# Performance work log

Hardware: AMD Instinct MI355X
Metric: run time of the kernel (lower is better)

## Reference

```python
import jax, jax.numpy as jnp
import numpy as np

N_HEAD = 32
N_QUERY_GROUPS = 8
HEAD_SIZE = 128
N_EMBD = 4096


def apply_rope(x, cos, sin):
    # x: [B, H, T, D]; cos/sin: [T, D] (rotary_percentage = 1.0 so D = head_size)
    d = x.shape[-1]
    x1, x2 = x[..., : d // 2], x[..., d // 2:]
    rotated = jnp.concatenate([-x2, x1], axis=-1)
    return x * cos + rotated * sin


def setup_inputs() -> dict:
    key = jax.random.key(0)
    k1, k2, k3, k4, k5 = jax.random.split(key, 5)
    B, T = 1, 2048
    x = jax.random.normal(k1, (B, T, N_EMBD), dtype=jnp.float32)
    # realistic rope angles
    theta = 10000.0 ** (-jnp.arange(0, HEAD_SIZE // 2, dtype=jnp.float32) * 2.0 / HEAD_SIZE)
    ang = jnp.arange(T, dtype=jnp.float32)[:, None] * theta[None, :]
    ang = jnp.concatenate([ang, ang], axis=-1)  # [T, HEAD_SIZE]
    cos, sin = jnp.cos(ang), jnp.sin(ang)
    qkv_dim = (N_HEAD + 2 * N_QUERY_GROUPS) * HEAD_SIZE  # 6144
    w_attn = jax.random.normal(k2, (qkv_dim, N_EMBD), dtype=jnp.float32) * (N_EMBD ** -0.5)
    w_proj = jax.random.normal(k3, (N_EMBD, N_HEAD * HEAD_SIZE), dtype=jnp.float32) * ((N_HEAD * HEAD_SIZE) ** -0.5)
    return {"x": x, "cos": cos, "sin": sin, "w_attn": w_attn, "w_proj": w_proj}


def reference(x, cos, sin, w_attn, w_proj):
    B, T, C = x.shape
    G, hs = N_QUERY_GROUPS, HEAD_SIZE
    q_per_kv = N_HEAD // G  # 4
    total_qkv = q_per_kv + 2

    qkv = jnp.einsum('btc,oc->bto', x, w_attn)  # [B, T, 6144]
    qkv = qkv.reshape(B, T, G, total_qkv, hs).transpose(0, 2, 3, 1, 4)  # [B, G, total, T, hs]
    q = qkv[:, :, :q_per_kv]              # [B, G, qpk, T, hs]
    k = qkv[:, :, q_per_kv:q_per_kv + 1]  # [B, G, 1,   T, hs]
    v = qkv[:, :, q_per_kv + 1:]          # [B, G, 1,   T, hs]

    # GQA expand to per-query heads, then flatten head dims
    k = jnp.broadcast_to(k, (B, G, q_per_kv, T, hs))
    v = jnp.broadcast_to(v, (B, G, q_per_kv, T, hs))
    q = q.reshape(B, N_HEAD, T, hs)
    k = k.reshape(B, N_HEAD, T, hs)
    v = v.reshape(B, N_HEAD, T, hs)

    # rotary_percentage = 1.0 -> rope over full head dim
    q = apply_rope(q, cos, sin)
    k = apply_rope(k, cos, sin)

    scale = 1.0 / jnp.sqrt(jnp.float32(hs))
    scores = jnp.einsum('bhqd,bhkd->bhqk', q, k) * scale  # [B, H, T, T]
    causal = jnp.tril(jnp.ones((T, T), dtype=bool))
    scores = jnp.where(causal, scores, jnp.finfo(scores.dtype).min)
    attn = jax.nn.softmax(scores, axis=-1)
    y = jnp.einsum('bhqk,bhkd->bhqd', attn, v)  # [B, H, T, hs]
    y = y.transpose(0, 2, 1, 3).reshape(B, T, N_HEAD * hs)
    return jnp.einsum('bto,co->btc', y, w_proj)  # [B, T, C]
```

## Files before the change

### kernel.cpp

```cpp
#include <hip/hip_runtime.h>
#include <hip/hip_bf16.h>

typedef __attribute__((ext_vector_type(8))) short short8;
typedef __attribute__((ext_vector_type(4))) float f32x4;

__device__ inline unsigned short f2bf(float f) {
  __hip_bfloat16 h = __float2bfloat16(f);
  return *reinterpret_cast<unsigned short*>(&h);
}
__device__ inline float bf2f(unsigned short u) {
  union { unsigned u; float f; } v; v.u = ((unsigned)u) << 16;
  return v.f;
}

#define GLOAD_LDS16(g, l)                                          \
  __builtin_amdgcn_global_load_lds(                                \
      (const __attribute__((address_space(1))) void*)(g),          \
      (__attribute__((address_space(3))) void*)(l), 16, 0, 0)

#define MFMA16(a, b, c) __builtin_amdgcn_mfma_f32_16x16x32_bf16((a), (b), (c), 0, 0, 0)

#define LGKM0()                                              \
  asm volatile("s_waitcnt lgkmcnt(0)" ::: "memory");         \
  __builtin_amdgcn_sched_barrier(0);

__global__ void f32_to_bf16(const float* __restrict__ in,
                            unsigned short* __restrict__ out, int n8) {
  int i = blockIdx.x * 256 + threadIdx.x;
  if (i >= n8) return;
  const float4* p = (const float4*)in + (size_t)i * 2;
  float4 a = p[0], b = p[1];
  short8 v;
  v[0] = f2bf(a.x); v[1] = f2bf(a.y); v[2] = f2bf(a.z); v[3] = f2bf(a.w);
  v[4] = f2bf(b.x); v[5] = f2bf(b.y); v[6] = f2bf(b.z); v[7] = f2bf(b.w);
  *((short8*)out + i) = v;
}

__global__ __launch_bounds__(512, 2)
void gemm_qkv(const unsigned short* __restrict__ A, const unsigned short* __restrict__ B,
              unsigned short* __restrict__ C, int M, int N, int K) {
  __shared__ __align__(16) unsigned short lds[2][448 * 64];
  const int t = threadIdx.x, lane = t & 63, w = t >> 6;
  const int wm = w >> 2, wn = w & 3;
  const int r16 = lane & 15, kg = lane >> 4;
  const int bm = blockIdx.x & 7, bn = blockIdx.x >> 3;
  const int NT = K >> 6;
  const int sr = lane >> 3, sch = lane & 7;
  const unsigned short* Ag = A + (size_t)(bm * 256) * K;
  const unsigned short* Bg = B + (size_t)(bn * 192) * K;

  auto stA = [&](int kt, int j, int b) {
    int rl = j * 64 + w * 8 + sr, sc = sch ^ (rl & 7);
    GLOAD_LDS16(Ag + (size_t)rl * K + kt * 64 + sc * 8, &lds[b][(j * 64 + w * 8) * 64]);
  };
  auto stB = [&](int kt, int j, int b) {
    int rl = j * 64 + w * 8 + sr, sc = sch ^ (rl & 7);
    GLOAD_LDS16(Bg + (size_t)rl * K + kt * 64 + sc * 8, &lds[b][(256 + j * 64 + w * 8) * 64]);
  };
  auto lda = [&](int b, int m, int kk) -> short8 {
    int row = wm * 128 + m * 16 + r16, ch = (kk * 4 + kg) ^ (row & 7);
    return *(const short8*)__builtin_assume_aligned(&lds[b][row * 64 + ch * 8], 16);
  };
  auto ldb = [&](int b, int n, int kk) -> short8 {
    int row = wn * 48 + n * 16 + r16, ch = (kk * 4 + kg) ^ (row & 7);
    return *(const short8*)__builtin_assume_aligned(&lds[b][(256 + row) * 64 + ch * 8], 16);
  };

  f32x4 acc[8][3] = {};
  short8 a0[4][2], a1[4][2], bb[3][2];

#pragma unroll
  for (int j = 0; j < 4; ++j) stA(0, j, 0);
#pragma unroll
  for (int j = 0; j < 3; ++j) stB(0, j, 0);
#pragma unroll
  for (int j = 0; j < 3; ++j) stA(1, j, 1);
#pragma unroll
  for (int j = 0; j < 3; ++j) stB(1, j, 1);
  asm volatile("s_waitcnt vmcnt(6)" ::: "memory");
  __builtin_amdgcn_sched_barrier(0);
  __builtin_amdgcn_s_barrier();

  for (int kt = 0; kt < NT; ++kt) {
    const int b = kt & 1;
    const bool pf1 = kt + 1 < NT, pf2 = kt + 2 < NT;

    if (pf1) stA(kt + 1, 3, b ^ 1);
#pragma unroll
    for (int m = 0; m < 4; ++m) { a0[m][0] = lda(b, m, 0); a0[m][1] = lda(b, m, 1); }
#pragma unroll
    for (int n = 0; n < 2; ++n) { bb[n][0] = ldb(b, n, 0); bb[n][1] = ldb(b, n, 1); }
    __builtin_amdgcn_s_barrier();
    LGKM0();
    __builtin_amdgcn_s_setprio(1);
#pragma unroll
    for (int m = 0; m < 4; ++m)
#pragma unroll
      for (int n = 0; n < 2; ++n)
#pragma unroll
        for (int kk = 0; kk < 2; ++kk) acc[m][n] = MFMA16(a0[m][kk], bb[n][kk], acc[m][n]);
    __builtin_amdgcn_s_setprio(0);
    __builtin_amdgcn_s_barrier();

    bb[2][0] = ldb(b, 2, 0); bb[2][1] = ldb(b, 2, 1);
#pragma unroll
    for (int m = 0; m < 4; ++m) { a1[m][0] = lda(b, 4 + m, 0); a1[m][1] = lda(b, 4 + m, 1); }
    if (pf2) { stA(kt + 2, 0, b); stA(kt + 2, 2, b); }
    __builtin_amdgcn_s_barrier();
    LGKM0();
    __builtin_amdgcn_s_setprio(1);
#pragma unroll
    for (int m = 0; m < 4; ++m)
#pragma unroll
      for (int kk = 0; kk < 2; ++kk) acc[m][2] = MFMA16(a0[m][kk], bb[2][kk], acc[m][2]);
#pragma unroll
    for (int m = 0; m < 4; ++m)
#pragma unroll
      for (int kk = 0; kk < 2; ++kk) acc[4 + m][2] = MFMA16(a1[m][kk], bb[2][kk], acc[4 + m][2]);
    __builtin_amdgcn_s_setprio(0);
    __builtin_amdgcn_s_barrier();

    if (pf2) { stB(kt + 2, 0, b); stB(kt + 2, 1, b); stB(kt + 2, 2, b); stA(kt + 2, 1, b); }
    __builtin_amdgcn_s_barrier();
    __builtin_amdgcn_s_setprio(1);
#pragma unroll
    for (int m = 0; m < 4; ++m)
#pragma unroll
      for (int n = 0; n < 2; ++n)
#pragma unroll
        for (int kk = 0; kk < 2; ++kk) acc[4 + m][n] = MFMA16(a1[m][kk], bb[n][kk], acc[4 + m][n]);
    __builtin_amdgcn_s_setprio(0);
    if (pf1) {
      if (pf2) asm volatile("s_waitcnt vmcnt(6)" ::: "memory");
      else     asm volatile("s_waitcnt vmcnt(0)" ::: "memory");
      __builtin_amdgcn_sched_barrier(0);
      __builtin_amdgcn_s_barrier();
    }
  }

#pragma unroll
  for (int m = 0; m < 8; ++m)
#pragma unroll
    for (int n = 0; n < 3; ++n)
#pragma unroll
      for (int j = 0; j < 4; ++j) {
        int row = bm * 256 + wm * 128 + m * 16 + kg * 4 + j;
        int col = bn * 192 + wn * 48 + n * 16 + r16;
        C[(size_t)row * N + col] = f2bf(acc[m][n][j]);
      }
}

__global__ __launch_bounds__(512, 2)
void gemm_proj(const unsigned short* __restrict__ A, const unsigned short* __restrict__ B,
               float* __restrict__ C, int M, int N, int K) {
  __shared__ __align__(16) unsigned short lds[2][384 * 64];
  const int t = threadIdx.x, lane = t & 63, w = t >> 6;
  const int wm = w >> 2, wn = w & 3;
  const int r16 = lane & 15, kg = lane >> 4;
  const int bm = blockIdx.x & 15, bn = blockIdx.x >> 4;
  const int NT = K >> 6;
  const int sr = lane >> 3, sch = lane & 7;
  const unsigned short* Ag = A + (size_t)(bm * 128) * K;
  const unsigned short* Bg = B + (size_t)(bn * 256) * K;

  auto stA = [&](int kt, int j, int b) {
    int rl = j * 64 + w * 8 + sr, sc = sch ^ (rl & 7);
    GLOAD_LDS16(Ag + (size_t)rl * K + kt * 64 + sc * 8, &lds[b][(j * 64 + w * 8) * 64]);
  };
  auto stB = [&](int kt, int j, int b) {
    int rl = j * 64 + w * 8 + sr, sc = sch ^ (rl & 7);
    GLOAD_LDS16(Bg + (size_t)rl * K + kt * 64 + sc * 8, &lds[b][(128 + j * 64 + w * 8) * 64]);
  };
  auto lda = [&](int b, int m, int kk) -> short8 {
    int row = wm * 64 + m * 16 + r16, ch = (kk * 4 + kg) ^ (row & 7);
    return *(const short8*)__builtin_assume_aligned(&lds[b][row * 64 + ch * 8], 16);
  };
  auto ldb = [&](int b, int n, int kk) -> short8 {
    int row = wn * 64 + n * 16 + r16, ch = (kk * 4 + kg) ^ (row & 7);
    return *(const short8*)__builtin_assume_aligned(&lds[b][(128 + row) * 64 + ch * 8], 16);
  };

  f32x4 acc[4][4] = {};
  short8 af[4][2], bb[4][2];

#pragma unroll
  for (int j = 0; j < 2; ++j) stA(0, j, 0);
#pragma unroll
  for (int j = 0; j < 4; ++j) stB(0, j, 0);
#pragma unroll
  for (int j = 0; j < 2; ++j) stA(1, j, 1);
  asm volatile("s_waitcnt vmcnt(2)" ::: "memory");
  __builtin_amdgcn_sched_barrier(0);
  __builtin_amdgcn_s_barrier();

  for (int kt = 0; kt < NT; ++kt) {
    const int b = kt & 1;
    const bool pf1 = kt + 1 < NT, pf2 = kt + 2 < NT;

    if (pf1) { stB(kt + 1, 0, b ^ 1); stB(kt + 1, 1, b ^ 1); stB(kt + 1, 2, b ^ 1); stB(kt + 1, 3, b ^ 1); }
#pragma unroll
    for (int m = 0; m < 4; ++m) { af[m][0] = lda(b, m, 0); af[m][1] = lda(b, m, 1); }
#pragma unroll
    for (int n = 0; n < 2; ++n) { bb[n][0] = ldb(b, n, 0); bb[n][1] = ldb(b, n, 1); }
    __builtin_amdgcn_s_barrier();
    LGKM0();
    __builtin_amdgcn_s_setprio(1);
#pragma unroll
    for (int m = 0; m < 4; ++m)
#pragma unroll
      for (int n = 0; n < 2; ++n)
#pragma unroll
        for (int kk = 0; kk < 2; ++kk) acc[m][n] = MFMA16(af[m][kk], bb[n][kk], acc[m][n]);
    __builtin_amdgcn_s_setprio(0);
    __builtin_amdgcn_s_barrier();

#pragma unroll
    for (int n = 2; n < 4; ++n) { bb[n][0] = ldb(b, n, 0); bb[n][1] = ldb(b, n, 1); }
    if (pf2) { stA(kt + 2, 0, b); stA(kt + 2, 1, b); }
    __builtin_amdgcn_s_barrier();
    LGKM0();
    __builtin_amdgcn_s_setprio(1);
#pragma unroll
    for (int m = 0; m < 4; ++m)
#pragma unroll
      for (int n = 2; n < 4; ++n)
#pragma unroll
        for (int kk = 0; kk < 2; ++kk) acc[m][n] = MFMA16(af[m][kk], bb[n][kk], acc[m][n]);
    __builtin_amdgcn_s_setprio(0);
    if (pf1) {
      if (pf2) asm volatile("s_waitcnt vmcnt(2)" ::: "memory");
      else     asm volatile("s_waitcnt vmcnt(0)" ::: "memory");
      __builtin_amdgcn_sched_barrier(0);
      __builtin_amdgcn_s_barrier();
    }
  }

#pragma unroll
  for (int m = 0; m < 4; ++m)
#pragma unroll
    for (int n = 0; n < 4; ++n)
#pragma unroll
      for (int j = 0; j < 4; ++j) {
        int row = bm * 128 + wm * 64 + m * 16 + kg * 4 + j;
        int col = bn * 256 + wn * 64 + n * 16 + r16;
        C[(size_t)row * N + col] = acc[m][n][j];
      }
}

__global__ void rope_qk(const unsigned short* __restrict__ qkv,
                        const float* __restrict__ cosb, const float* __restrict__ sinb,
                        unsigned short* __restrict__ Q, unsigned short* __restrict__ K) {
  int pair = blockIdx.x * 4 + (threadIdx.x >> 6);
  int l = threadIdx.x & 63;
  int t = pair / 40, slot = pair - t * 40;
  const unsigned short* src;
  unsigned short* dst;
  float scale;
  if (slot < 32) {
    int g = slot >> 2, j = slot & 3;
    src = qkv + (size_t)t * 6144 + g * 768 + j * 128;
    dst = Q + ((size_t)slot * 2048 + t) * 128;
    scale = 0.08838834764831845f;
  } else {
    int g = slot - 32;
    src = qkv + (size_t)t * 6144 + g * 768 + 512;
    dst = K + ((size_t)g * 2048 + t) * 128;
    scale = 1.0f;
  }
  float x1 = bf2f(src[l]), x2 = bf2f(src[64 + l]);
  float c1 = cosb[t * 128 + l], s1 = sinb[t * 128 + l];
  float c2 = cosb[t * 128 + 64 + l], s2 = sinb[t * 128 + 64 + l];
  dst[l]      = f2bf((x1 * c1 - x2 * s1) * scale);
  dst[64 + l] = f2bf((x2 * c2 + x1 * s2) * scale);
}

__global__ void transpose_v(const unsigned short* __restrict__ qkv,
                            unsigned short* __restrict__ Vt) {
  __shared__ __align__(16) unsigned short tile[64][136];
  int g = blockIdx.y, t0 = blockIdx.x * 64;
  int th = threadIdx.x;
  int r = th >> 2, c0 = (th & 3) * 32;
  const unsigned short* src = qkv + (size_t)(t0 + r) * 6144 + g * 768 + 640 + c0;
#pragma unroll
  for (int i = 0; i < 4; ++i)
    *(short8*)&tile[r][c0 + i * 8] = *(const short8*)(src + i * 8);
  __syncthreads();
  int d = th >> 1, tc = (th & 1) * 32;
  unsigned short* dst = Vt + (size_t)(g * 128 + d) * 2048 + t0 + tc;
#pragma unroll
  for (int j = 0; j < 32; ++j) dst[j] = tile[tc + j][d];
}

__global__ __launch_bounds__(256, 2)
void flash_attn(const unsigned short* __restrict__ Q, const unsigned short* __restrict__ K,
                const unsigned short* __restrict__ Vt, unsigned short* __restrict__ Y) {
  __shared__ __align__(16) unsigned short Ksm[2][64 * 128];
  __shared__ __align__(16) unsigned short Vsm[2][128 * 64];

  const int h = blockIdx.y, g = h >> 2;
  const int t = threadIdx.x, lane = t & 63, w = t >> 6;
  const int r16 = lane & 15, kg = lane >> 4;
  const bool odd = kg & 1;
  const bool hi = kg >> 1;
  const bool useswap = odd ^ hi;

  const unsigned short* Kg = K + (size_t)g * 2048 * 128;
  const unsigned short* Vg = Vt + (size_t)g * 128 * 2048;

  const int krl = lane >> 4, kc = lane & 15;
  const int vrl = lane >> 3, vc = lane & 7;

  auto stage = [&](int kvs, int b) {
#pragma unroll
    for (int i = 0; i < 4; ++i) {
      int row = w * 16 + i * 4 + krl;
      int sc = kc ^ (row & 7);
      GLOAD_LDS16(Kg + (size_t)(kvs + row) * 128 + sc * 8,
                  &Ksm[b][(w * 16 + i * 4) * 128]);
    }
#pragma unroll
    for (int i = 0; i < 4; ++i) {
      int d = w * 32 + i * 8 + vrl;
      int sc = vc ^ (d & 7);
      GLOAD_LDS16(Vg + (size_t)d * 2048 + kvs + sc * 8,
                  &Vsm[b][(w * 32 + i * 8) * 64]);
    }
  };

  auto process = [&](int q0) {
    short8 qf[4];
    const unsigned short* qrow = Q + ((size_t)h * 2048 + q0 + w * 16 + r16) * 128;
#pragma unroll
    for (int kk = 0; kk < 4; ++kk) qf[kk] = *(const short8*)(qrow + kk * 32 + kg * 8);

    f32x4 o[8] = {};
    float mrow = -1e30f, lrow = 0.f;
    const int qg = q0 + w * 16 + r16;
    const int nt = q0 / 64 + 1;

    __syncthreads();
    stage(0, 0);

    for (int kt = 0; kt < nt; ++kt) {
      const int b = kt & 1;
      const int kv0 = kt * 64;
      __syncthreads();
      if (kt + 1 < nt) stage((kt + 1) * 64, b ^ 1);

      f32x4 s[4] = {};
      __builtin_amdgcn_s_setprio(1);
#pragma unroll
      for (int n = 0; n < 4; ++n) {
        int kr = n * 16 + r16;
#pragma unroll
        for (int kk = 0; kk < 4; ++kk) {
          short8 kf = *(const short8*)__builtin_assume_aligned(
              &Ksm[b][kr * 128 + ((kk * 32 + kg * 8) ^ ((kr & 7) << 3))], 16);
          s[n] = __builtin_amdgcn_mfma_f32_16x16x32_bf16(kf, qf[kk], s[n], 0, 0, 0);
        }
      }
      __builtin_amdgcn_s_setprio(0);

      if (kv0 + 63 > q0 + w * 16) {
#pragma unroll
        for (int n = 0; n < 4; ++n)
#pragma unroll
          for (int j = 0; j < 4; ++j)
            if (kv0 + n * 16 + kg * 4 + j > qg) s[n][j] = -1e30f;
      }

      float rmax = -1e30f;
#pragma unroll
      for (int n = 0; n < 4; ++n)
#pragma unroll
        for (int j = 0; j < 4; ++j) rmax = fmaxf(rmax, s[n][j]);
      rmax = fmaxf(rmax, __shfl_xor(rmax, 16));
      rmax = fmaxf(rmax, __shfl_xor(rmax, 32));

      if (__builtin_amdgcn_ballot_w64(rmax > mrow)) {
        float mnew = fmaxf(mrow, rmax);
        float fac = __expf(mrow - mnew);
        mrow = mnew;
        lrow *= fac;
        float fj[4];
#pragma unroll
        for (int j = 0; j < 4; ++j) fj[j] = __shfl(fac, kg * 4 + j);
#pragma unroll
        for (int f = 0; f < 8; ++f)
#pragma unroll
          for (int j = 0; j < 4; ++j) o[f][j] *= fj[j];
      }

      float p[4][4];
      float rs = 0.f;
#pragma unroll
      for (int n = 0; n < 4; ++n)
#pragma unroll
        for (int j = 0; j < 4; ++j) {
          p[n][j] = __expf(s[n][j] - mrow);
          rs += p[n][j];
        }
      rs += __shfl_xor(rs, 16);
      rs += __shfl_xor(rs, 32);
      lrow += rs;

      unsigned bpk[4][2], xpk[4][2];
#pragma unroll
      for (int n = 0; n < 4; ++n)
#pragma unroll
        for (int i = 0; i < 2; ++i)
          bpk[n][i] = (unsigned)f2bf(p[n][2 * i]) | ((unsigned)f2bf(p[n][2 * i + 1]) << 16);
#pragma unroll
      for (int n = 0; n < 4; ++n)
#pragma unroll
        for (int i = 0; i < 2; ++i) xpk[n][i] = __shfl_xor(bpk[n][i], 16);

      unsigned pl[4][2], ph[4][2];
#pragma unroll
      for (int n = 0; n < 4; ++n)
#pragma unroll
        for (int i = 0; i < 2; ++i) {
          pl[n][i] = odd ? xpk[n][i] : bpk[n][i];
          ph[n][i] = odd ? bpk[n][i] : xpk[n][i];
        }

      short8 pa[2];
#pragma unroll
      for (int kk = 0; kk < 2; ++kk) {
        unsigned kp0 = hi ? pl[2 * kk + 1][0] : pl[2 * kk][0];
        unsigned kp1 = hi ? pl[2 * kk + 1][1] : pl[2 * kk][1];
        unsigned kp2 = hi ? ph[2 * kk + 1][0] : ph[2 * kk][0];
        unsigned kp3 = hi ? ph[2 * kk + 1][1] : ph[2 * kk][1];
        unsigned sd0 = hi ? pl[2 * kk][0] : pl[2 * kk + 1][0];
        unsigned sd1 = hi ? pl[2 * kk][1] : pl[2 * kk + 1][1];
        unsigned sd2 = hi ? ph[2 * kk][0] : ph[2 * kk + 1][0];
        unsigned sd3 = hi ? ph[2 * kk][1] : ph[2 * kk + 1][1];
        unsigned g0 = __shfl_xor(sd0, 32), g1 = __shfl_xor(sd1, 32);
        unsigned g2 = __shfl_xor(sd2, 32), g3 = __shfl_xor(sd3, 32);
        union { unsigned u[4]; short8 v; } pu;
        pu.u[0] = useswap ? g0 : kp0;
        pu.u[1] = useswap ? g1 : kp1;
        pu.u[2] = useswap ? g2 : kp2;
        pu.u[3] = useswap ? g3 : kp3;
        pa[kk] = pu.v;
      }

      __builtin_amdgcn_s_setprio(1);
#pragma unroll
      for (int kk = 0; kk < 2; ++kk) {
#pragma unroll
        for (int f = 0; f < 8; ++f) {
          int d = f * 16 + r16;
          short8 vf = *(const short8*)__builtin_assume_aligned(
              &Vsm[b][d * 64 + ((kk * 32 + kg * 8) ^ ((d & 7) << 3))], 16);
          o[f] = __builtin_amdgcn_mfma_f32_16x16x32_bf16(pa[kk], vf, o[f], 0, 0, 0);
        }
      }
      __builtin_amdgcn_s_setprio(0);
    }

    float inv = 1.f / lrow;
    float invj[4];
#pragma unroll
    for (int j = 0; j < 4; ++j) invj[j] = __shfl(inv, kg * 4 + j);
#pragma unroll
    for (int j = 0; j < 4; ++j) {
      int row = q0 + w * 16 + kg * 4 + j;
      unsigned short* yr = Y + (size_t)row * 4096 + h * 128;
#pragma unroll
      for (int f = 0; f < 8; ++f) yr[f * 16 + r16] = f2bf(o[f][j] * invj[j]);
    }
  };

  const int pr = blockIdx.x;
  process(pr * 64);
  process((31 - pr) * 64);
}

extern "C" void kernel_launch(void* const* d_in, const int* in_sizes, int n_in,
                              void* d_out, int out_size, void* d_ws, size_t ws_size,
                              hipStream_t stream) {
  const float* x      = (const float*)d_in[0];
  const float* cosb   = (const float*)d_in[1];
  const float* sinb   = (const float*)d_in[2];
  const float* w_attn = (const float*)d_in[3];
  const float* w_proj = (const float*)d_in[4];
  float* out = (float*)d_out;

  char* ws = (char*)d_ws;
  const size_t MB = 1024 * 1024;
  unsigned short* Xb  = (unsigned short*)(ws);
  unsigned short* Wa  = (unsigned short*)(ws + 16 * MB);
  unsigned short* Wp  = (unsigned short*)(ws);
  unsigned short* Qb  = (unsigned short*)(ws + 32 * MB);
  unsigned short* Kb  = (unsigned short*)(ws + 48 * MB);
  unsigned short* Vt  = (unsigned short*)(ws + 52 * MB);
  unsigned short* qkv = (unsigned short*)(ws + 64 * MB);
  unsigned short* Yb  = (unsigned short*)(ws + 64 * MB);

  f32_to_bf16<<<4096, 256, 0, stream>>>(x, Xb, 2048 * 4096 / 8);
  f32_to_bf16<<<12288, 256, 0, stream>>>(w_attn, Wa, 6144 * 4096 / 8);
  gemm_qkv<<<256, 512, 0, stream>>>(Xb, Wa, qkv, 2048, 6144, 4096);
  rope_qk<<<20480, 256, 0, stream>>>(qkv, cosb, sinb, Qb, Kb);
  transpose_v<<<dim3(32, 8), 256, 0, stream>>>(qkv, Vt);
  f32_to_bf16<<<8192, 256, 0, stream>>>(w_proj, Wp, 4096 * 4096 / 8);
  flash_attn<<<dim3(16, 32), 256, 0, stream>>>(Qb, Kb, Vt, Yb);
  gemm_proj<<<256, 512, 0, stream>>>(Yb, Wp, out, 2048, 4096, 4096);
}
```

Measured before the change: 315.5 us.

## Merge conversions, restructure QKV GEMM pipeline, one q-tile per flash block

Replaces three fp32-to-bf16 conversion launches with a single grid-stride kernel and moves Wp and Yb to non-aliasing workspace regions. Reworks the QKV GEMM main loop into two compute phases per k-tile with a different prefetch schedule. Changes flash attention to one 64-row query tile per block with single-buffered K/V and higher occupancy (launch bounds 4). Each block is now launched longest-first, relying on the hardware scheduler rather than paired tiles for balance, and loses K/V double buffering overlap.

After: 351.7 us. 1.11x slower.

```diff
diff --git a/kernel.cpp b/kernel.cpp
--- a/kernel.cpp
+++ b/kernel.cpp
@@ -24,16 +24,23 @@
   asm volatile("s_waitcnt lgkmcnt(0)" ::: "memory");         \
   __builtin_amdgcn_sched_barrier(0);
 
-__global__ void f32_to_bf16(const float* __restrict__ in,
-                            unsigned short* __restrict__ out, int n8) {
-  int i = blockIdx.x * 256 + threadIdx.x;
-  if (i >= n8) return;
-  const float4* p = (const float4*)in + (size_t)i * 2;
-  float4 a = p[0], b = p[1];
-  short8 v;
-  v[0] = f2bf(a.x); v[1] = f2bf(a.y); v[2] = f2bf(a.z); v[3] = f2bf(a.w);
-  v[4] = f2bf(b.x); v[5] = f2bf(b.y); v[6] = f2bf(b.z); v[7] = f2bf(b.w);
-  *((short8*)out + i) = v;
+__global__ void cvt3(const float* __restrict__ x, const float* __restrict__ wa,
+                     const float* __restrict__ wp, unsigned short* __restrict__ Xb,
+                     unsigned short* __restrict__ Wa, unsigned short* __restrict__ Wp) {
+  const int N_X = 1048576, N_WA = 3145728;
+  const int TOT = 6291456;
+  for (int i = blockIdx.x * 256 + threadIdx.x; i < TOT; i += gridDim.x * 256) {
+    const float* src; unsigned short* dst; int off;
+    if (i < N_X)            { src = x;  dst = Xb; off = i; }
+    else if (i < N_X + N_WA){ src = wa; dst = Wa; off = i - N_X; }
+    else                    { src = wp; dst = Wp; off = i - N_X - N_WA; }
+    const float4* p = (const float4*)src + (size_t)off * 2;
+    float4 a = p[0], b = p[1];
+    short8 v;
+    v[0] = f2bf(a.x); v[1] = f2bf(a.y); v[2] = f2bf(a.z); v[3] = f2bf(a.w);
+    v[4] = f2bf(b.x); v[5] = f2bf(b.y); v[6] = f2bf(b.z); v[7] = f2bf(b.w);
+    *((short8*)dst + off) = v;
+  }
 }
 
 __global__ __launch_bounds__(512, 2)
@@ -74,10 +81,9 @@
 #pragma unroll
   for (int j = 0; j < 3; ++j) stB(0, j, 0);
 #pragma unroll
-  for (int j = 0; j < 3; ++j) stA(1, j, 1);
-#pragma unroll
   for (int j = 0; j < 3; ++j) stB(1, j, 1);
-  asm volatile("s_waitcnt vmcnt(6)" ::: "memory");
+  stA(1, 0, 1); stA(1, 2, 1);
+  asm volatile("s_waitcnt vmcnt(5)" ::: "memory");
   __builtin_amdgcn_sched_barrier(0);
   __builtin_amdgcn_s_barrier();
 
@@ -85,53 +91,38 @@
     const int b = kt & 1;
     const bool pf1 = kt + 1 < NT, pf2 = kt + 2 < NT;
 
-    if (pf1) stA(kt + 1, 3, b ^ 1);
+    if (pf1) { stA(kt + 1, 1, b ^ 1); stA(kt + 1, 3, b ^ 1); }
 #pragma unroll
     for (int m = 0; m < 4; ++m) { a0[m][0] = lda(b, m, 0); a0[m][1] = lda(b, m, 1); }
 #pragma unroll
-    for (int n = 0; n < 2; ++n) { bb[n][0] = ldb(b, n, 0); bb[n][1] = ldb(b, n, 1); }
+    for (int n = 0; n < 3; ++n) { bb[n][0] = ldb(b, n, 0); bb[n][1] = ldb(b, n, 1); }
     __builtin_amdgcn_s_barrier();
     LGKM0();
     __builtin_amdgcn_s_setprio(1);
 #pragma unroll
     for (int m = 0; m < 4; ++m)
 #pragma unroll
-      for (int n = 0; n < 2; ++n)
+      for (int n = 0; n < 3; ++n)
 #pragma unroll
         for (int kk = 0; kk < 2; ++kk) acc[m][n] = MFMA16(a0[m][kk], bb[n][kk], acc[m][n]);
     __builtin_amdgcn_s_setprio(0);
     __builtin_amdgcn_s_barrier();
 
-    bb[2][0] = ldb(b, 2, 0); bb[2][1] = ldb(b, 2, 1);
+    if (pf2) { stB(kt + 2, 0, b); stB(kt + 2, 1, b); stB(kt + 2, 2, b); stA(kt + 2, 0, b); stA(kt + 2, 2, b); }
 #pragma unroll
     for (int m = 0; m < 4; ++m) { a1[m][0] = lda(b, 4 + m, 0); a1[m][1] = lda(b, 4 + m, 1); }
-    if (pf2) { stA(kt + 2, 0, b); stA(kt + 2, 2, b); }
     __builtin_amdgcn_s_barrier();
     LGKM0();
     __builtin_amdgcn_s_setprio(1);
 #pragma unroll
     for (int m = 0; m < 4; ++m)
 #pragma unroll
-      for (int kk = 0; kk < 2; ++kk) acc[m][2] = MFMA16(a0[m][kk], bb[2][kk], acc[m][2]);
-#pragma unroll
-    for (int m = 0; m < 4; ++m)
-#pragma unroll
-      for (int kk = 0; kk < 2; ++kk) acc[4 + m][2] = MFMA16(a1[m][kk], bb[2][kk], acc[4 + m][2]);
-    __builtin_amdgcn_s_setprio(0);
-    __builtin_amdgcn_s_barrier();
-
-    if (pf2) { stB(kt + 2, 0, b); stB(kt + 2, 1, b); stB(kt + 2, 2, b); stA(kt + 2, 1, b); }
-    __builtin_amdgcn_s_barrier();
-    __builtin_amdgcn_s_setprio(1);
-#pragma unroll
-    for (int m = 0; m < 4; ++m)
-#pragma unroll
-      for (int n = 0; n < 2; ++n)
+      for (int n = 0; n < 3; ++n)
 #pragma unroll
         for (int kk = 0; kk < 2; ++kk) acc[4 + m][n] = MFMA16(a1[m][kk], bb[n][kk], acc[4 + m][n]);
     __builtin_amdgcn_s_setprio(0);
     if (pf1) {
-      if (pf2) asm volatile("s_waitcnt vmcnt(6)" ::: "memory");
+      if (pf2) asm volatile("s_waitcnt vmcnt(5)" ::: "memory");
       else     asm volatile("s_waitcnt vmcnt(0)" ::: "memory");
       __builtin_amdgcn_sched_barrier(0);
       __builtin_amdgcn_s_barrier();
@@ -291,13 +282,15 @@
   for (int j = 0; j < 32; ++j) dst[j] = tile[tc + j][d];
 }
 
-__global__ __launch_bounds__(256, 2)
+__global__ __launch_bounds__(256, 4)
 void flash_attn(const unsigned short* __restrict__ Q, const unsigned short* __restrict__ K,
                 const unsigned short* __restrict__ Vt, unsigned short* __restrict__ Y) {
-  __shared__ __align__(16) unsigned short Ksm[2][64 * 128];
-  __shared__ __align__(16) unsigned short Vsm[2][128 * 64];
+  __shared__ __align__(16) unsigned short Ksm[64 * 128];
+  __shared__ __align__(16) unsigned short Vsm[128 * 64];
 
   const int h = blockIdx.y, g = h >> 2;
+  const int qi = 31 - (int)blockIdx.x;
+  const int q0 = qi * 64;
   const int t = threadIdx.x, lane = t & 63, w = t >> 6;
   const int r16 = lane & 15, kg = lane >> 4;
   const bool odd = kg & 1;
@@ -310,171 +303,162 @@
   const int krl = lane >> 4, kc = lane & 15;
   const int vrl = lane >> 3, vc = lane & 7;
 
-  auto stage = [&](int kvs, int b) {
+  auto stage = [&](int kvs) {
 #pragma unroll
     for (int i = 0; i < 4; ++i) {
       int row = w * 16 + i * 4 + krl;
       int sc = kc ^ (row & 7);
       GLOAD_LDS16(Kg + (size_t)(kvs + row) * 128 + sc * 8,
-                  &Ksm[b][(w * 16 + i * 4) * 128]);
+                  &Ksm[(w * 16 + i * 4) * 128]);
     }
 #pragma unroll
     for (int i = 0; i < 4; ++i) {
       int d = w * 32 + i * 8 + vrl;
       int sc = vc ^ (d & 7);
       GLOAD_LDS16(Vg + (size_t)d * 2048 + kvs + sc * 8,
-                  &Vsm[b][(w * 32 + i * 8) * 64]);
-    }
-  };
-
-  auto process = [&](int q0) {
-    short8 qf[4];
-    const unsigned short* qrow = Q + ((size_t)h * 2048 + q0 + w * 16 + r16) * 128;
-#pragma unroll
-    for (int kk = 0; kk < 4; ++kk) qf[kk] = *(const short8*)(qrow + kk * 32 + kg * 8);
-
-    f32x4 o[8] = {};
-    float mrow = -1e30f, lrow = 0.f;
-    const int qg = q0 + w * 16 + r16;
-    const int nt = q0 / 64 + 1;
-
+                  &Vsm[(w * 32 + i * 8) * 64]);
+    }
+  };
+
+  short8 qf[4];
+  const unsigned short* qrow = Q + ((size_t)h * 2048 + q0 + w * 16 + r16) * 128;
+#pragma unroll
+  for (int kk = 0; kk < 4; ++kk) qf[kk] = *(const short8*)(qrow + kk * 32 + kg * 8);
+
+  f32x4 o[8] = {};
+  float mrow = -1e30f, lrow = 0.f;
+  const int qg = q0 + w * 16 + r16;
+  const int nt = qi + 1;
+
+  for (int kt = 0; kt < nt; ++kt) {
+    const int kv0 = kt * 64;
+    stage(kv0);
     __syncthreads();
-    stage(0, 0);
-
-    for (int kt = 0; kt < nt; ++kt) {
-      const int b = kt & 1;
-      const int kv0 = kt * 64;
-      __syncthreads();
-      if (kt + 1 < nt) stage((kt + 1) * 64, b ^ 1);
-
-      f32x4 s[4] = {};
-      __builtin_amdgcn_s_setprio(1);
-#pragma unroll
-      for (int n = 0; n < 4; ++n) {
-        int kr = n * 16 + r16;
-#pragma unroll
-        for (int kk = 0; kk < 4; ++kk) {
-          short8 kf = *(const short8*)__builtin_assume_aligned(
-              &Ksm[b][kr * 128 + ((kk * 32 + kg * 8) ^ ((kr & 7) << 3))], 16);
-          s[n] = __builtin_amdgcn_mfma_f32_16x16x32_bf16(kf, qf[kk], s[n], 0, 0, 0);
-        }
-      }
-      __builtin_amdgcn_s_setprio(0);
-
-      if (kv0 + 63 > q0 + w * 16) {
-#pragma unroll
-        for (int n = 0; n < 4; ++n)
-#pragma unroll
-          for (int j = 0; j < 4; ++j)
-            if (kv0 + n * 16 + kg * 4 + j > qg) s[n][j] = -1e30f;
-      }
-
-      float rmax = -1e30f;
+
+    f32x4 s[4] = {};
+    __builtin_amdgcn_s_setprio(1);
+#pragma unroll
+    for (int n = 0; n < 4; ++n) {
+      int kr = n * 16 + r16;
+#pragma unroll
+      for (int kk = 0; kk < 4; ++kk) {
+        short8 kf = *(const short8*)__builtin_assume_aligned(
+            &Ksm[kr * 128 + ((kk * 32 + kg * 8) ^ ((kr & 7) << 3))], 16);
+        s[n] = __builtin_amdgcn_mfma_f32_16x16x32_bf16(kf, qf[kk], s[n], 0, 0, 0);
+      }
+    }
+    __builtin_amdgcn_s_setprio(0);
+
+    if (kv0 + 63 > q0 + w * 16) {
 #pragma unroll
       for (int n = 0; n < 4; ++n)
 #pragma unroll
-        for (int j = 0; j < 4; ++j) rmax = fmaxf(rmax, s[n][j]);
-      rmax = fmaxf(rmax, __shfl_xor(rmax, 16));
-      rmax = fmaxf(rmax, __shfl_xor(rmax, 32));
-
-      if (__builtin_amdgcn_ballot_w64(rmax > mrow)) {
-        float mnew = fmaxf(mrow, rmax);
-        float fac = __expf(mrow - mnew);
-        mrow = mnew;
-        lrow *= fac;
-        float fj[4];
-#pragma unroll
-        for (int j = 0; j < 4; ++j) fj[j] = __shfl(fac, kg * 4 + j);
-#pragma unroll
-        for (int f = 0; f < 8; ++f)
-#pragma unroll
-          for (int j = 0; j < 4; ++j) o[f][j] *= fj[j];
-      }
-
-      float p[4][4];
-      float rs = 0.f;
-#pragma unroll
-      for (int n = 0; n < 4; ++n)
-#pragma unroll
-        for (int j = 0; j < 4; ++j) {
-          p[n][j] = __expf(s[n][j] - mrow);
-          rs += p[n][j];
-        }
-      rs += __shfl_xor(rs, 16);
-      rs += __shfl_xor(rs, 32);
-      lrow += rs;
-
-      unsigned bpk[4][2], xpk[4][2];
-#pragma unroll
-      for (int n = 0; n < 4; ++n)
-#pragma unroll
-        for (int i = 0; i < 2; ++i)
-          bpk[n][i] = (unsigned)f2bf(p[n][2 * i]) | ((unsigned)f2bf(p[n][2 * i + 1]) << 16);
-#pragma unroll
-      for (int n = 0; n < 4; ++n)
-#pragma unroll
-        for (int i = 0; i < 2; ++i) xpk[n][i] = __shfl_xor(bpk[n][i], 16);
-
-      unsigned pl[4][2], ph[4][2];
-#pragma unroll
-      for (int n = 0; n < 4; ++n)
-#pragma unroll
-        for (int i = 0; i < 2; ++i) {
-          pl[n][i] = odd ? xpk[n][i] : bpk[n][i];
-          ph[n][i] = odd ? bpk[n][i] : xpk[n][i];
-        }
-
-      short8 pa[2];
-#pragma unroll
-      for (int kk = 0; kk < 2; ++kk) {
-        unsigned kp0 = hi ? pl[2 * kk + 1][0] : pl[2 * kk][0];
-        unsigned kp1 = hi ? pl[2 * kk + 1][1] : pl[2 * kk][1];
-        unsigned kp2 = hi ? ph[2 * kk + 1][0] : ph[2 * kk][0];
-        unsigned kp3 = hi ? ph[2 * kk + 1][1] : ph[2 * kk][1];
-        unsigned sd0 = hi ? pl[2 * kk][0] : pl[2 * kk + 1][0];
-        unsigned sd1 = hi ? pl[2 * kk][1] : pl[2 * kk + 1][1];
-        unsigned sd2 = hi ? ph[2 * kk][0] : ph[2 * kk + 1][0];
-        unsigned sd3 = hi ? ph[2 * kk][1] : ph[2 * kk + 1][1];
-        unsigned g0 = __shfl_xor(sd0, 32), g1 = __shfl_xor(sd1, 32);
-        unsigned g2 = __shfl_xor(sd2, 32), g3 = __shfl_xor(sd3, 32);
-        union { unsigned u[4]; short8 v; } pu;
-        pu.u[0] = useswap ? g0 : kp0;
-        pu.u[1] = useswap ? g1 : kp1;
-        pu.u[2] = useswap ? g2 : kp2;
-        pu.u[3] = useswap ? g3 : kp3;
-        pa[kk] = pu.v;
-      }
-
-      __builtin_amdgcn_s_setprio(1);
-#pragma unroll
-      for (int kk = 0; kk < 2; ++kk) {
-#pragma unroll
-        for (int f = 0; f < 8; ++f) {
-          int d = f * 16 + r16;
-          short8 vf = *(const short8*)__builtin_assume_aligned(
-              &Vsm[b][d * 64 + ((kk * 32 + kg * 8) ^ ((d & 7) << 3))], 16);
-          o[f] = __builtin_amdgcn_mfma_f32_16x16x32_bf16(pa[kk], vf, o[f], 0, 0, 0);
-        }
-      }
-      __builtin_amdgcn_s_setprio(0);
-    }
-
-    float inv = 1.f / lrow;
-    float invj[4];
-#pragma unroll
-    for (int j = 0; j < 4; ++j) invj[j] = __shfl(inv, kg * 4 + j);
-#pragma unroll
-    for (int j = 0; j < 4; ++j) {
-      int row = q0 + w * 16 + kg * 4 + j;
-      unsigned short* yr = Y + (size_t)row * 4096 + h * 128;
-#pragma unroll
-      for (int f = 0; f < 8; ++f) yr[f * 16 + r16] = f2bf(o[f][j] * invj[j]);
-    }
-  };
-
-  const int pr = blockIdx.x;
-  process(pr * 64);
-  process((31 - pr) * 64);
+        for (int j = 0; j < 4; ++j)
+          if (kv0 + n * 16 + kg * 4 + j > qg) s[n][j] = -1e30f;
+    }
+
+    float rmax = -1e30f;
+#pragma unroll
+    for (int n = 0; n < 4; ++n)
+#pragma unroll
+      for (int j = 0; j < 4; ++j) rmax = fmaxf(rmax, s[n][j]);
+    rmax = fmaxf(rmax, __shfl_xor(rmax, 16));
+    rmax = fmaxf(rmax, __shfl_xor(rmax, 32));
+
+    if (__builtin_amdgcn_ballot_w64(rmax > mrow)) {
+      float mnew = fmaxf(mrow, rmax);
+      float fac = __expf(mrow - mnew);
+      mrow = mnew;
+      lrow *= fac;
+      float fj[4];
+#pragma unroll
+      for (int j = 0; j < 4; ++j) fj[j] = __shfl(fac, kg * 4 + j);
+#pragma unroll
+      for (int f = 0; f < 8; ++f)
+#pragma unroll
+        for (int j = 0; j < 4; ++j) o[f][j] *= fj[j];
+    }
+
+    float p[4][4];
+    float rs = 0.f;
+#pragma unroll
+    for (int n = 0; n < 4; ++n)
+#pragma unroll
+      for (int j = 0; j < 4; ++j) {
+        p[n][j] = __expf(s[n][j] - mrow);
+        rs += p[n][j];
+      }
+    rs += __shfl_xor(rs, 16);
+    rs += __shfl_xor(rs, 32);
+    lrow += rs;
+
+    unsigned bpk[4][2], xpk[4][2];
+#pragma unroll
+    for (int n = 0; n < 4; ++n)
+#pragma unroll
+      for (int i = 0; i < 2; ++i)
+        bpk[n][i] = (unsigned)f2bf(p[n][2 * i]) | ((unsigned)f2bf(p[n][2 * i + 1]) << 16);
+#pragma unroll
+    for (int n = 0; n < 4; ++n)
+#pragma unroll
+      for (int i = 0; i < 2; ++i) xpk[n][i] = __shfl_xor(bpk[n][i], 16);
+
+    unsigned pl[4][2], ph[4][2];
+#pragma unroll
+    for (int n = 0; n < 4; ++n)
+#pragma unroll
+      for (int i = 0; i < 2; ++i) {
+        pl[n][i] = odd ? xpk[n][i] : bpk[n][i];
+        ph[n][i] = odd ? bpk[n][i] : xpk[n][i];
+      }
+
+    short8 pa[2];
+#pragma unroll
+    for (int kk = 0; kk < 2; ++kk) {
+      unsigned kp0 = hi ? pl[2 * kk + 1][0] : pl[2 * kk][0];
+      unsigned kp1 = hi ? pl[2 * kk + 1][1] : pl[2 * kk][1];
+      unsigned kp2 = hi ? ph[2 * kk + 1][0] : ph[2 * kk][0];
+      unsigned kp3 = hi ? ph[2 * kk + 1][1] : ph[2 * kk][1];
+      unsigned sd0 = hi ? pl[2 * kk][0] : pl[2 * kk + 1][0];
+      unsigned sd1 = hi ? pl[2 * kk][1] : pl[2 * kk + 1][1];
+      unsigned sd2 = hi ? ph[2 * kk][0] : ph[2 * kk + 1][0];
+      unsigned sd3 = hi ? ph[2 * kk][1] : ph[2 * kk + 1][1];
+      unsigned g0 = __shfl_xor(sd0, 32), g1 = __shfl_xor(sd1, 32);
+      unsigned g2 = __shfl_xor(sd2, 32), g3 = __shfl_xor(sd3, 32);
+      union { unsigned u[4]; short8 v; } pu;
+      pu.u[0] = useswap ? g0 : kp0;
+      pu.u[1] = useswap ? g1 : kp1;
+      pu.u[2] = useswap ? g2 : kp2;
+      pu.u[3] = useswap ? g3 : kp3;
+      pa[kk] = pu.v;
+    }
+
+    __builtin_amdgcn_s_setprio(1);
+#pragma unroll
+    for (int kk = 0; kk < 2; ++kk) {
+#pragma unroll
+      for (int f = 0; f < 8; ++f) {
+        int d = f * 16 + r16;
+        short8 vf = *(const short8*)__builtin_assume_aligned(
+            &Vsm[d * 64 + ((kk * 32 + kg * 8) ^ ((d & 7) << 3))], 16);
+        o[f] = __builtin_amdgcn_mfma_f32_16x16x32_bf16(pa[kk], vf, o[f], 0, 0, 0);
+      }
+    }
+    __builtin_amdgcn_s_setprio(0);
+    __syncthreads();
+  }
+
+  float inv = 1.f / lrow;
+  float invj[4];
+#pragma unroll
+  for (int j = 0; j < 4; ++j) invj[j] = __shfl(inv, kg * 4 + j);
+#pragma unroll
+  for (int j = 0; j < 4; ++j) {
+    int row = q0 + w * 16 + kg * 4 + j;
+    unsigned short* yr = Y + (size_t)row * 4096 + h * 128;
+#pragma unroll
+    for (int f = 0; f < 8; ++f) yr[f * 16 + r16] = f2bf(o[f][j] * invj[j]);
+  }
 }
 
 extern "C" void kernel_launch(void* const* d_in, const int* in_sizes, int n_in,
@@ -491,19 +475,17 @@
   const size_t MB = 1024 * 1024;
   unsigned short* Xb  = (unsigned short*)(ws);
   unsigned short* Wa  = (unsigned short*)(ws + 16 * MB);
-  unsigned short* Wp  = (unsigned short*)(ws);
+  unsigned short* Wp  = (unsigned short*)(ws + 112 * MB);
   unsigned short* Qb  = (unsigned short*)(ws + 32 * MB);
   unsigned short* Kb  = (unsigned short*)(ws + 48 * MB);
   unsigned short* Vt  = (unsigned short*)(ws + 52 * MB);
   unsigned short* qkv = (unsigned short*)(ws + 64 * MB);
-  unsigned short* Yb  = (unsigned short*)(ws + 64 * MB);
-
-  f32_to_bf16<<<4096, 256, 0, stream>>>(x, Xb, 2048 * 4096 / 8);
-  f32_to_bf16<<<12288, 256, 0, stream>>>(w_attn, Wa, 6144 * 4096 / 8);
+  unsigned short* Yb  = (unsigned short*)(ws + 88 * MB);
+
+  cvt3<<<2048, 256, 0, stream>>>(x, w_attn, w_proj, Xb, Wa, Wp);
   gemm_qkv<<<256, 512, 0, stream>>>(Xb, Wa, qkv, 2048, 6144, 4096);
   rope_qk<<<20480, 256, 0, stream>>>(qkv, cosb, sinb, Qb, Kb);
   transpose_v<<<dim3(32, 8), 256, 0, stream>>>(qkv, Vt);
-  f32_to_bf16<<<8192, 256, 0, stream>>>(w_proj, Wp, 4096 * 4096 / 8);
-  flash_attn<<<dim3(16, 32), 256, 0, stream>>>(Qb, Kb, Vt, Yb);
+  flash_attn<<<dim3(32, 32), 256, 0, stream>>>(Qb, Kb, Vt, Yb);
   gemm_proj<<<256, 512, 0, stream>>>(Yb, Wp, out, 2048, 4096, 4096);
 }
```
